# Kernel tuning notes

Measured on AMD Instinct MI355X. Metric: run time of the kernel, lower is better.

Reference implementation:

```python
import jax, jax.numpy as jnp
import numpy as np

NUM_EMBEDDINGS = 8192
EMBEDDING_DIM = 256
COMMITMENT_COST = 0.25


def setup_inputs() -> dict:
    key = jax.random.key(0)
    k1, k2 = jax.random.split(key)
    inputs = jax.random.normal(k1, (16, EMBEDDING_DIM, 32, 32), dtype=jnp.float32)
    # codebook initialized uniform(-1/K, 1/K) as in the torch module
    emb = jax.random.uniform(k2, (NUM_EMBEDDINGS, EMBEDDING_DIM), dtype=jnp.float32,
                             minval=-1.0 / NUM_EMBEDDINGS, maxval=1.0 / NUM_EMBEDDINGS)
    return {"inputs": inputs, "emb": emb}


def reference(inputs, emb):
    B, C, H, W = inputs.shape  # C == EMBEDDING_DIM
    flat = inputs.transpose(0, 2, 3, 1).reshape(-1, C)  # [N, D]
    # squared L2 distances to every codeword: [N, K]
    d = (jnp.sum(flat * flat, axis=1, keepdims=True)
         + jnp.sum(emb * emb, axis=1)
         - 2.0 * (flat @ emb.T))
    idx = jnp.argmin(d, axis=1)  # [N]
    # gather lookup (same math as one-hot @ emb)
    q = emb[idx].reshape(B, H, W, C).transpose(0, 3, 1, 2)  # [B, C, H, W]
    q_latent_loss = jnp.mean((jax.lax.stop_gradient(q) - inputs) ** 2)
    e_latent_loss = jnp.mean((q - jax.lax.stop_gradient(inputs)) ** 2)
    loss = q_latent_loss + COMMITMENT_COST * e_latent_loss
    # straight-through estimator
    q_st = inputs + jax.lax.stop_gradient(q - inputs)
    return q_st, loss, idx[:, None]
```

## Files before the change

kernel.cpp:

```cpp
#include <hip/hip_runtime.h>
#include <hip/hip_fp16.h>

#define NROWS 16384
#define KCB   8192
#define DIM   256
#define HW    1024

typedef __attribute__((ext_vector_type(8))) short  bf16x8;
typedef __attribute__((ext_vector_type(4))) float  f32x4;

#define WS_XT    16384
#define WS_XB    (WS_XT + 4194304)
#define WS_EB    (WS_XB + 2097152)
#define WS_TMAX  (WS_EB + 1048576)

#define GLD_LDS(g, l) __builtin_amdgcn_global_load_lds( \
    (const __attribute__((address_space(1))) void*)(g), \
    (__attribute__((address_space(3))) void*)(l), 16, 0, 0)

__device__ inline unsigned short f2bf(float v) {
  unsigned u = __float_as_uint(v);
  unsigned r = (u + 0x7FFFu + ((u >> 16) & 1u)) >> 16;
  return (unsigned short)r;
}

__device__ inline int dperm(int d, int row) {
  return (d & ~63) | ((((d >> 3) + row) & 7) << 3) | (d & 7);
}

__device__ inline unsigned long long shfl_xor_u64(unsigned long long v, int off) {
  unsigned lo = (unsigned)v, hi = (unsigned)(v >> 32);
  lo = __shfl_xor(lo, off, 64);
  hi = __shfl_xor(hi, off, 64);
  return ((unsigned long long)hi << 32) | lo;
}

__device__ float xsq_exact(const float* __restrict__ xr) {
#pragma clang fp contract(off)
  float halves[2];
#pragma unroll
  for (int h = 0; h < 2; ++h) {
    float r[8];
#pragma unroll
    for (int j = 0; j < 8; ++j) {
      const float a = xr[h * 128 + j];
      r[j] = a * a;
    }
    for (int i = 8; i < 128; i += 8) {
#pragma unroll
      for (int j = 0; j < 8; ++j) {
        const float a = xr[h * 128 + i + j];
        const float sq = a * a;
        r[j] = r[j] + sq;
      }
    }
    halves[h] = ((r[0] + r[1]) + (r[2] + r[3])) + ((r[4] + r[5]) + (r[6] + r[7]));
  }
  return halves[0] + halves[1];
}

__global__ __launch_bounds__(256) void vq_prep(const float* __restrict__ x,
                                               const float* __restrict__ emb,
                                               float* __restrict__ xT,
                                               unsigned short* __restrict__ xb,
                                               unsigned short* __restrict__ eb) {
  __shared__ float lds[64 * 68];
  const int bid = blockIdx.x;
  const int t = threadIdx.x;
  const int w = t >> 6, lane = t & 63;
  if (bid < 1024) {
    const int b = bid & 15, d0 = ((bid >> 4) & 3) * 64, hw0 = (bid >> 6) * 64;
    const int u = lane >> 4, l15 = lane & 15;
#pragma unroll
    for (int it = 0; it < 4; ++it) {
      const int dl = it * 16 + w * 4 + u;
      const int hb = l15 * 4;
      const float4 v =
          *(const float4*)&x[((size_t)(b * DIM + d0 + dl)) * HW + hw0 + hb];
      const int slot = (it * 4 + w) ^ l15;
      lds[(hb + 0) * 68 + slot * 4 + u] = v.x;
      lds[(hb + 1) * 68 + slot * 4 + u] = v.y;
      lds[(hb + 2) * 68 + slot * 4 + u] = v.z;
      lds[(hb + 3) * 68 + slot * 4 + u] = v.w;
    }
    __syncthreads();
#pragma unroll
    for (int it = 0; it < 4; ++it) {
      const int nl = it * 16 + w * 4 + u;
      const int slot = (it * 4 + w) ^ l15;
      const float4 f = *(const float4*)&lds[nl * 68 + slot * 4];
      const int n = b * HW + hw0 + nl;
      const int d = d0 + l15 * 4;
      *(float4*)&xT[(size_t)n * DIM + d] = f;
      ushort4 o;
      o.x = f2bf(f.x); o.y = f2bf(f.y); o.z = f2bf(f.z); o.w = f2bf(f.w);
      const int dp = d0 + ((((d >> 3) + n) & 7) << 3) + (d & 7);
      *(ushort4*)&xb[(size_t)n * DIM + dp] = o;
    }
  } else {
#pragma unroll
    for (int c = 0; c < 4; ++c) {
      const int i = ((bid - 1024) * 1024 + c * 256 + t) * 4;
      const int k = i >> 8, d = i & 255;
      const float4 v = *(const float4*)&emb[i];
      ushort4 o;
      o.x = f2bf(v.x); o.y = f2bf(v.y); o.z = f2bf(v.z); o.w = f2bf(v.w);
      *(ushort4*)&eb[(size_t)k * DIM + dperm(d, k)] = o;
    }
  }
}

__global__ __launch_bounds__(256, 4) void vq_coarse(const unsigned short* __restrict__ xb,
                                                    const unsigned short* __restrict__ eb,
                                                    __half* __restrict__ tmax) {
  __shared__ __align__(16) unsigned short a_lds[128 * 64];
  __shared__ __align__(16) unsigned short b_lds[128 * 64];
  const int lin = blockIdx.x;
  const int xcd = lin & 7;
  const int s_  = lin >> 3;
  const int row_t = xcd * 16 + (s_ & 15);
  const int col_t = s_ >> 4;
  const int t = threadIdx.x, lane = t & 63, w = t >> 6;
  const int wr = w >> 1, wc = w & 1;
  const int row0 = row_t * 128, col0 = col_t * 128;
  const int q = lane >> 4, l15 = lane & 15;
  const int srow = lane >> 3, scol = (lane & 7) * 8;

  const unsigned short* agp = xb + (size_t)(row0 + srow) * DIM + scol;
  const unsigned short* bgp = eb + (size_t)(col0 + srow) * DIM + scol;

  f32x4 acc[4][4];
#pragma unroll
  for (int i = 0; i < 4; ++i)
#pragma unroll
    for (int j = 0; j < 4; ++j) acc[i][j] = (f32x4){0.f, 0.f, 0.f, 0.f};

  for (int kc = 0; kc < 4; ++kc) {
    const int k0 = kc * 64;
    __syncthreads();
#pragma unroll
    for (int c = 0; c < 4; ++c) {
      const int rbase = c * 32 + w * 8;
      GLD_LDS(agp + (size_t)rbase * DIM + k0, &a_lds[rbase * 64]);
      GLD_LDS(bgp + (size_t)rbase * DIM + k0, &b_lds[rbase * 64]);
    }
    __syncthreads();
#pragma unroll
    for (int s = 0; s < 2; ++s) {
      bf16x8 af[4], bfr[4];
#pragma unroll
      for (int i = 0; i < 4; ++i)
        af[i] = *(const bf16x8*)
            &a_lds[(wr * 64 + i * 16 + l15) * 64 + (((s * 4 + q + l15) & 7) << 3)];
#pragma unroll
      for (int j = 0; j < 4; ++j)
        bfr[j] = *(const bf16x8*)
            &b_lds[(wc * 64 + j * 16 + l15) * 64 + (((s * 4 + q + l15) & 7) << 3)];
#pragma unroll
      for (int i = 0; i < 4; ++i)
#pragma unroll
        for (int j = 0; j < 4; ++j)
          acc[i][j] = __builtin_amdgcn_mfma_f32_16x16x32_bf16(af[i], bfr[j], acc[i][j], 0, 0, 0);
    }
  }

#pragma unroll
  for (int i = 0; i < 4; ++i) {
#pragma unroll
    for (int r = 0; r < 4; ++r) {
      float mx = fmaxf(fmaxf(acc[i][0][r], acc[i][1][r]),
                       fmaxf(acc[i][2][r], acc[i][3][r]));
      mx = fmaxf(mx, __shfl_xor(mx, 1, 64));
      if ((l15 & 1) == 0) {
        const int row = row0 + wr * 64 + i * 16 + q * 4 + r;
        tmax[(size_t)row * 1024 + (col_t * 2 + wc) * 8 + (l15 >> 1)] = __float2half(mx);
      }
    }
  }
}

#define DELTA 1.0e-4f
#define MAXT  768
__global__ __launch_bounds__(256) void vq_select(const float* __restrict__ xT,
                                                 const float* __restrict__ emb,
                                                 const __half* __restrict__ tmax,
                                                 float* __restrict__ out_q,
                                                 float* __restrict__ out_idx,
                                                 float* __restrict__ lpart) {
  __shared__ int tasks[4][MAXT + 16];
  __shared__ __align__(16) float x_sh[4][8][260];
  __shared__ float xsq_sh[4][8];
  __shared__ int bestk_sh[32];
  __shared__ float wsum_sh[4];
  const int t = threadIdx.x, lane = t & 63, w = t >> 6;
  const int n8 = (blockIdx.x * 4 + w) * 8;

#pragma unroll
  for (int r = 0; r < 8; ++r)
    GLD_LDS(xT + (size_t)(n8 + r) * DIM + lane * 4, &x_sh[w][r][0]);

  int cnt = 0;
  const int jj8 = lane & 7;
  for (int r = 0; r < 8; ++r) {
    float v[2][8];
#pragma unroll
    for (int it = 0; it < 2; ++it) {
      union { uint4 u; __half h[8]; } U;
      U.u = *(const uint4*)((const char*)tmax + (size_t)(n8 + r) * 2048 + it * 1024 + lane * 16);
#pragma unroll
      for (int u = 0; u < 8; ++u) v[it][u] = __half2float(U.h[u]);
    }
    float m = v[0][0];
#pragma unroll
    for (int it = 0; it < 2; ++it)
#pragma unroll
      for (int u = 0; u < 8; ++u) m = fmaxf(m, v[it][u]);
#pragma unroll
    for (int off = 1; off < 64; off <<= 1) m = fmaxf(m, __shfl_xor(m, off, 64));
    const float thr = m - DELTA;
#pragma unroll
    for (int it = 0; it < 2; ++it)
#pragma unroll
      for (int u = 0; u < 8; ++u) {
        unsigned long long mask = __ballot(v[it][u] >= thr);
        while (mask) {
          const int b = __builtin_ctzll(mask);
          mask &= mask - 1;
          const int e = it * 512 + b * 8 + u;
          const int blkI = e >> 3, wi = e & 7;
          const int col = blkI * 64 + (jj8 >> 1) * 16 + wi * 2 + (jj8 & 1);
          if (cnt < MAXT) tasks[w][cnt + jj8] = (r << 16) | col;
          cnt += 8;
        }
      }
  }
  const int total = (cnt < MAXT) ? cnt : MAXT;

  __syncthreads();

  if (lane < 8) xsq_sh[w][lane] = xsq_exact(&x_sh[w][lane][0]);

  unsigned long long best[8];
#pragma unroll
  for (int r = 0; r < 8; ++r) best[r] = 0xFFFFFFFFFFFFFFFFull;

  for (int base = 0; base < total; base += 192) {
    int rr[3], cc[3];
    bool val[3];
#pragma unroll
    for (int c = 0; c < 3; ++c) {
      const int idx = base + lane + 64 * c;
      const int tk = (idx < total) ? tasks[w][idx] : tasks[w][0];
      val[c] = (idx < total);
      rr[c] = tk >> 16;
      cc[c] = tk & 0xFFFF;
    }
    const float4* e0 = (const float4*)(emb + (size_t)cc[0] * DIM);
    const float4* e1 = (const float4*)(emb + (size_t)cc[1] * DIM);
    const float4* e2 = (const float4*)(emb + (size_t)cc[2] * DIM);
    const float* x0 = &x_sh[w][0][0] + rr[0] * 260;
    const float* x1 = &x_sh[w][0][0] + rr[1] * 260;
    const float* x2 = &x_sh[w][0][0] + rr[2] * 260;
    float a0 = 0.f, a1 = 0.f, a2 = 0.f;
#pragma unroll 4
    for (int d4 = 0; d4 < 64; ++d4) {
      const float4 ee0 = e0[d4], xx0 = *(const float4*)(x0 + d4 * 4);
      const float4 ee1 = e1[d4], xx1 = *(const float4*)(x1 + d4 * 4);
      const float4 ee2 = e2[d4], xx2 = *(const float4*)(x2 + d4 * 4);
      a0 = fmaf(xx0.x, ee0.x, a0); a0 = fmaf(xx0.y, ee0.y, a0);
      a0 = fmaf(xx0.z, ee0.z, a0); a0 = fmaf(xx0.w, ee0.w, a0);
      a1 = fmaf(xx1.x, ee1.x, a1); a1 = fmaf(xx1.y, ee1.y, a1);
      a1 = fmaf(xx1.z, ee1.z, a1); a1 = fmaf(xx1.w, ee1.w, a1);
      a2 = fmaf(xx2.x, ee2.x, a2); a2 = fmaf(xx2.y, ee2.y, a2);
      a2 = fmaf(xx2.z, ee2.z, a2); a2 = fmaf(xx2.w, ee2.w, a2);
    }
    const float av[3] = {a0, a1, a2};
#pragma unroll
    for (int c = 0; c < 3; ++c) {
      if (val[c]) {
        const float sc = xsq_sh[w][rr[c]] - 2.0f * av[c];
        const unsigned long long pk =
            ((unsigned long long)__float_as_uint(sc) << 32) | (unsigned)cc[c];
#pragma unroll
        for (int r = 0; r < 8; ++r)
          if (rr[c] == r && pk < best[r]) best[r] = pk;
      }
    }
  }

#pragma unroll
  for (int r = 0; r < 8; ++r) {
    unsigned long long u = best[r];
#pragma unroll
    for (int off = 1; off < 64; off <<= 1) {
      const unsigned long long o = shfl_xor_u64(u, off);
      if (o < u) u = o;
    }
    if (lane == r) {
      const int col = (int)(u & 0xFFFFFFFFull);
      bestk_sh[w * 8 + r] = col;
      out_idx[n8 + r] = (float)col;
    }
  }

  __syncthreads();

  const int n0 = blockIdx.x * 32;
  const int b = n0 >> 10, hw0 = n0 & 1023;
  const int er = t & 31, dg = t >> 5;
  const int ks = bestk_sh[er];
  const float* eq = emb + (size_t)ks * DIM;
  const float* xrow = &x_sh[er >> 3][er & 7][0];
  float* op = out_q + (size_t)b * (DIM * HW) + hw0 + er;
  float lacc = 0.f;
#pragma unroll 4
  for (int it = 0; it < 32; ++it) {
    const int d = dg + 8 * it;
    const float qv = eq[d];
    const float xv = xrow[d];
    op[(size_t)d * HW] = qv;
    const float df = qv - xv;
    lacc = fmaf(df, df, lacc);
  }
#pragma unroll
  for (int off = 32; off > 0; off >>= 1) lacc += __shfl_down(lacc, off, 64);
  if (lane == 0) wsum_sh[w] = lacc;
  __syncthreads();
  if (t == 0) lpart[blockIdx.x] = wsum_sh[0] + wsum_sh[1] + wsum_sh[2] + wsum_sh[3];
}

__global__ __launch_bounds__(256) void vq_loss(const float* __restrict__ lpart,
                                               float* __restrict__ out_loss) {
  __shared__ double dsum[4];
  const int t = threadIdx.x;
  double s = (double)lpart[t] + (double)lpart[t + 256];
#pragma unroll
  for (int off = 32; off > 0; off >>= 1) s += __shfl_down(s, off, 64);
  if ((t & 63) == 0) dsum[t >> 6] = s;
  __syncthreads();
  if (t == 0) {
    const double total = dsum[0] + dsum[1] + dsum[2] + dsum[3];
    out_loss[0] = (float)(total * 1.25 / 4194304.0);
  }
}

extern "C" void kernel_launch(void* const* d_in, const int* in_sizes, int n_in,
                              void* d_out, int out_size, void* d_ws, size_t ws_size,
                              hipStream_t stream) {
  const float* x   = (const float*)d_in[0];
  const float* emb = (const float*)d_in[1];
  float* out = (float*)d_out;
  float* ws  = (float*)d_ws;

  float*          lpart = ws;
  float*          xT    = ws + WS_XT;
  unsigned short* xb    = (unsigned short*)(ws + WS_XB);
  unsigned short* eb    = (unsigned short*)(ws + WS_EB);
  __half*         tmax  = (__half*)(ws + WS_TMAX);

  float* out_q    = out;
  float* out_loss = out + 4194304;
  float* out_idx  = out + 4194305;

  vq_prep<<<1536, 256, 0, stream>>>(x, emb, xT, xb, eb);
  vq_coarse<<<(NROWS / 128) * (KCB / 128), 256, 0, stream>>>(xb, eb, tmax);
  vq_select<<<NROWS / 32, 256, 0, stream>>>(xT, emb, tmax, out_q, out_idx, lpart);
  vq_loss<<<1, 256, 0, stream>>>(lpart, out_loss);
}
```

Baseline: 202.0 us.

## Use two-level hierarchical tile-max table to shrink candidate scan in select kernel

The GEMM epilogue now writes per-4-column-group maxima plus a per-64-column block maximum into a compact 640-entry row, instead of 1024 per-pair maxima. The select kernel reads only the 128 block maxima per row to find the threshold, then reads fine maxima only for surviving blocks before emitting candidate tasks in 16-column units. This cuts tmax memory traffic and the ballot/scan work per row. In exchange, each surviving unit now covers 16 columns instead of 8, so more candidates may be evaluated exactly, and the MAXT cap may be hit sooner.

```diff
diff --git a/kernel.cpp b/kernel.cpp
--- a/kernel.cpp
+++ b/kernel.cpp
@@ -13,6 +13,7 @@
 #define WS_XB    (WS_XT + 4194304)
 #define WS_EB    (WS_XB + 2097152)
 #define WS_TMAX  (WS_EB + 1048576)
+#define TMS      640
 
 #define GLD_LDS(g, l) __builtin_amdgcn_global_load_lds( \
     (const __attribute__((address_space(1))) void*)(g), \
@@ -164,6 +165,7 @@
     }
   }
 
+  const int blk = col_t * 2 + wc;
 #pragma unroll
   for (int i = 0; i < 4; ++i) {
 #pragma unroll
@@ -171,10 +173,14 @@
       float mx = fmaxf(fmaxf(acc[i][0][r], acc[i][1][r]),
                        fmaxf(acc[i][2][r], acc[i][3][r]));
       mx = fmaxf(mx, __shfl_xor(mx, 1, 64));
-      if ((l15 & 1) == 0) {
-        const int row = row0 + wr * 64 + i * 16 + q * 4 + r;
-        tmax[(size_t)row * 1024 + (col_t * 2 + wc) * 8 + (l15 >> 1)] = __float2half(mx);
-      }
+      mx = fmaxf(mx, __shfl_xor(mx, 2, 64));
+      const int row = row0 + wr * 64 + i * 16 + q * 4 + r;
+      if ((l15 & 3) == 0)
+        tmax[(size_t)row * TMS + blk * 4 + (l15 >> 2)] = __float2half(mx);
+      float m2 = fmaxf(mx, __shfl_xor(mx, 4, 64));
+      m2 = fmaxf(m2, __shfl_xor(m2, 8, 64));
+      if (l15 == 0)
+        tmax[(size_t)row * TMS + 512 + blk] = __float2half(m2);
     }
   }
 }
@@ -200,39 +206,38 @@
     GLD_LDS(xT + (size_t)(n8 + r) * DIM + lane * 4, &x_sh[w][r][0]);
 
   int cnt = 0;
-  const int jj8 = lane & 7;
-  for (int r = 0; r < 8; ++r) {
-    float v[2][8];
-#pragma unroll
-    for (int it = 0; it < 2; ++it) {
-      union { uint4 u; __half h[8]; } U;
-      U.u = *(const uint4*)((const char*)tmax + (size_t)(n8 + r) * 2048 + it * 1024 + lane * 16);
-#pragma unroll
-      for (int u = 0; u < 8; ++u) v[it][u] = __half2float(U.h[u]);
-    }
-    float m = v[0][0];
-#pragma unroll
-    for (int it = 0; it < 2; ++it)
-#pragma unroll
-      for (int u = 0; u < 8; ++u) m = fmaxf(m, v[it][u]);
+  const int jj = lane & 15;
+  for (int rI = 0; rI < 8; ++rI) {
+    const __half* trow = tmax + (size_t)(n8 + rI) * TMS;
+    union { unsigned u; __half h[2]; } B;
+    B.u = *(const unsigned*)((const char*)trow + 1024 + lane * 4);
+    const float b0 = __half2float(B.h[0]), b1 = __half2float(B.h[1]);
+    float m = fmaxf(b0, b1);
 #pragma unroll
     for (int off = 1; off < 64; off <<= 1) m = fmaxf(m, __shfl_xor(m, off, 64));
     const float thr = m - DELTA;
-#pragma unroll
-    for (int it = 0; it < 2; ++it)
-#pragma unroll
-      for (int u = 0; u < 8; ++u) {
-        unsigned long long mask = __ballot(v[it][u] >= thr);
-        while (mask) {
-          const int b = __builtin_ctzll(mask);
-          mask &= mask - 1;
-          const int e = it * 512 + b * 8 + u;
-          const int blkI = e >> 3, wi = e & 7;
-          const int col = blkI * 64 + (jj8 >> 1) * 16 + wi * 2 + (jj8 & 1);
-          if (cnt < MAXT) tasks[w][cnt + jj8] = (r << 16) | col;
-          cnt += 8;
+    unsigned long long mk0 = __ballot(b0 >= thr);
+    unsigned long long mk1 = __ballot(b1 >= thr);
+#pragma unroll
+    for (int pr = 0; pr < 2; ++pr) {
+      unsigned long long mk = pr ? mk1 : mk0;
+      while (mk) {
+        const int p = __builtin_ctzll(mk);
+        mk &= mk - 1;
+        const int blk = p * 2 + pr;
+        union { uint2 u; __half h[4]; } F;
+        F.u = *(const uint2*)((const char*)trow + blk * 8);
+        const float v4 = __half2float(F.h[lane & 3]);
+        unsigned units = (unsigned)(__ballot(v4 >= thr) & 0xFull);
+        while (units) {
+          const int r4 = __builtin_ctz(units);
+          units &= units - 1;
+          const int col = blk * 64 + (jj >> 2) * 16 + r4 * 4 + (jj & 3);
+          if (cnt < MAXT) tasks[w][cnt + jj] = (rI << 16) | col;
+          cnt += 16;
         }
       }
+    }
   }
   const int total = (cnt < MAXT) ? cnt : MAXT;
 
```

Result: slower. 261.6 us (+29.5%).
